# Performance work log

Hardware: AMD Instinct MI355X
Metric: run time of the kernel (lower is better)

Reference implementation:

```python
import jax, jax.numpy as jnp
import numpy as np
from math import factorial

LMAX = 5
MUL = 128            # multiplicity per irrep degree in the node embedding
NUM_CHANNELS = 4
NUM_RADII = 64
RES_BETA = 180
RES_ALPHA = 359
NUM_SPECIES = 5
NUM_GRAPHS = 16
NUM_NODES = 512
SH_DIM = (LMAX + 1) ** 2          # 36
EMB_DIM = MUL * SH_DIM            # 4608
NUM_IRREPS = MUL * (LMAX + 1)     # 768
INV_TEMP = 1.0


def _real_sh_basis(lmax, res_beta, res_alpha):
    """Orthonormal real spherical harmonics evaluated on a Gauss-Legendre beta grid
    and a uniform alpha grid (the grid used by e3nn.to_s2grid with gausslegendre
    quadrature). Returns B[(l*l + l + m), beta, alpha]. Precomputed in numpy since
    the grid is static."""
    y, _ = np.polynomial.legendre.leggauss(res_beta)          # y = cos(beta)
    alpha = np.linspace(0.0, 2.0 * np.pi, res_alpha, endpoint=False)
    # associated Legendre P[l, m] on y (Condon-Shortley phase)
    P = np.zeros((lmax + 1, lmax + 1, res_beta))
    P[0, 0] = 1.0
    somx2 = np.sqrt(np.clip(1.0 - y * y, 0.0, None))
    for m in range(1, lmax + 1):
        P[m, m] = -(2 * m - 1) * somx2 * P[m - 1, m - 1]
    for m in range(lmax):
        P[m + 1, m] = (2 * m + 1) * y * P[m, m]
    for m in range(lmax + 1):
        for l in range(m + 2, lmax + 1):
            P[l, m] = ((2 * l - 1) * y * P[l - 1, m] - (l + m - 1) * P[l - 2, m]) / (l - m)
    B = np.zeros(((lmax + 1) ** 2, res_beta, res_alpha))
    ones_a = np.ones_like(alpha)
    for l in range(lmax + 1):
        for m in range(l + 1):
            N = np.sqrt((2 * l + 1) / (4.0 * np.pi) * factorial(l - m) / factorial(l + m))
            if m == 0:
                B[l * l + l] = (N * P[l, 0])[:, None] * ones_a[None, :]
            else:
                B[l * l + l + m] = np.sqrt(2.0) * N * P[l, m][:, None] * np.cos(m * alpha)[None, :]
                B[l * l + l - m] = np.sqrt(2.0) * N * P[l, m][:, None] * np.sin(m * alpha)[None, :]
    return jnp.asarray(B, dtype=jnp.float32)


_B = _real_sh_basis(LMAX, RES_BETA, RES_ALPHA)   # (36, 180, 359)


def _split_blocks(emb):
    """Split an irreps array (G, sum_l MUL*(2l+1)) into per-degree blocks (G, MUL, 2l+1)."""
    blocks, off = [], 0
    for l in range(LMAX + 1):
        d = 2 * l + 1
        blocks.append(emb[:, off:off + MUL * d].reshape(-1, MUL, d))
        off += MUL * d
    return blocks


def setup_inputs() -> dict:
    key = jax.random.key(0)
    ks = jax.random.split(key, 13)
    inp = {
        "node_embeddings": jax.random.normal(ks[0], (NUM_NODES, EMB_DIM), jnp.float32),
        "species_embed": jax.random.normal(ks[1], (NUM_SPECIES, NUM_IRREPS), jnp.float32),
        "W_radial": jax.random.normal(ks[2], (MUL, NUM_RADII), jnp.float32),
        "W_mlp1": jax.random.normal(ks[3], (NUM_RADII, MUL), jnp.float32),
        "W_mlp2": jax.random.normal(ks[4], (MUL, NUM_RADII), jnp.float32),
    }
    for l in range(LMAX + 1):
        inp[f"W_ang_{l}"] = jax.random.normal(ks[5 + l], (MUL, NUM_CHANNELS), jnp.float32)
    inp["focus_indices"] = jax.random.randint(ks[11], (NUM_GRAPHS,), 0, NUM_NODES)
    inp["target_species"] = jax.random.randint(ks[12], (NUM_GRAPHS,), 0, NUM_SPECIES)
    return inp


def _forward(node_embeddings, species_embed, W_radial, W_mlp1, W_mlp2, W_ang,
             focus_indices, target_species):
    rsqrt_mul = np.float32(1.0 / np.sqrt(MUL))
    focus = node_embeddings[focus_indices]                 # (G, EMB_DIM)
    spec = species_embed[target_species]                   # (G, NUM_IRREPS), one scalar per irrep
    blocks = _split_blocks(focus)
    # target_species_embeddings * focus_node_embeddings: scale each irrep by its scalar
    scaled = [blk * spec[:, MUL * l:MUL * (l + 1), None] for l, blk in enumerate(blocks)]
    # radial path: e3nn Linear to num_radii x 0e (only 0e inputs contribute) + MLP
    scal0 = scaled[0][..., 0]                              # (G, MUL)
    r = (scal0 @ W_radial) * rsqrt_mul                     # (G, NUM_RADII)
    h = jax.nn.softplus((r @ W_mlp1) * np.float32(1.0 / np.sqrt(NUM_RADII)))
    radial_logits = (h @ W_mlp2) * rsqrt_mul               # (G, NUM_RADII)
    # angular path: e3nn Linear to num_channels * s2_irreps (per-degree channel mixing)
    ang = jnp.concatenate(
        [jnp.einsum("gkm,kc->gcm", scaled[l], W_ang[l]) * rsqrt_mul
         for l in range(LMAX + 1)], axis=-1)               # (G, C, 36)
    # joint distribution coefficients: radial logit adds to the l=0 coefficient
    joint0 = ang[:, :, None, :1] + radial_logits[:, None, :, None]     # (G, C, R, 1)
    rest = jnp.broadcast_to(ang[:, :, None, 1:],
                            (NUM_GRAPHS, NUM_CHANNELS, NUM_RADII, SH_DIM - 1))
    log_position_coeffs = jnp.concatenate([joint0, rest], axis=-1) * np.float32(INV_TEMP)
    # log_coeffs_to_logits: SH synthesis on the grid, then logsumexp over channels
    pos_grid = jnp.einsum("gcrk,kba->gcrba", log_position_coeffs, _B)
    position_logits = jax.nn.logsumexp(pos_grid, axis=1)   # (G, R, beta, alpha)
    ang_grid = jnp.einsum("gck,kba->gcba", ang, _B)
    angular_logits = jax.nn.logsumexp(ang_grid, axis=1, keepdims=True)  # (G, 1, beta, alpha)
    return log_position_coeffs, position_logits, angular_logits, radial_logits


def reference(node_embeddings, species_embed, W_radial, W_mlp1, W_mlp2,
              W_ang_0, W_ang_1, W_ang_2, W_ang_3, W_ang_4, W_ang_5,
              focus_indices, target_species):
    W_ang = [W_ang_0, W_ang_1, W_ang_2, W_ang_3, W_ang_4, W_ang_5]
    return _forward(node_embeddings, species_embed, W_radial, W_mlp1, W_mlp2, W_ang,
                    focus_indices, target_species)
```

## Files before the change

kernel.cpp:

```cpp
#include <hip/hip_runtime.h>
#include <math.h>

#define LMAX   5
#define MUL    128
#define NCH    4
#define NRAD   64
#define RBETA  180
#define RALPHA 359
#define NGRAPH 16
#define SH_DIM 36
#define EMB_DIM 4608
#define NIRR   768

#define GRID_BA (RBETA * RALPHA)
#define N_F4    (GRID_BA / 4)

#define OUT0_OFF 0
#define OUT1_OFF 147456
#define OUT2_OFF (147456 + 66170880)
#define OUT3_OFF (147456 + 66170880 + 1033920)


__global__ void k_nodes(double* __restrict__ y) {
    __shared__ double rcp[RBETA];
    const int n = RBETA;
    int tid = threadIdx.x;
    for (int k = tid; k < n; k += blockDim.x) rcp[k] = 1.0 / (double)(k + 1);
    __syncthreads();
    int i = tid;
    if (i >= n) return;
    const double PI = 3.14159265358979323846;
    double x = -cos(PI * (i + 0.75) / (n + 0.5));
    for (int it = 0; it < 6; ++it) {
        double p0 = 1.0, p1 = x;
        for (int k = 1; k < n; ++k) {
            double p2 = ((2.0 * k + 1.0) * x * p1 - (double)k * p0) * rcp[k];
            p0 = p1; p1 = p2;
        }
        double dp = n * (x * p1 - p0) / (x * x - 1.0);
        x -= p1 / dp;
    }
    y[i] = x;
}

__global__ __launch_bounds__(256)
void k_small(const float* __restrict__ ne, const float* __restrict__ sp,
             const float* __restrict__ wrad, const float* __restrict__ wm1,
             const float* __restrict__ wm2,
             const float* __restrict__ wa0, const float* __restrict__ wa1,
             const float* __restrict__ wa2, const float* __restrict__ wa3,
             const float* __restrict__ wa4, const float* __restrict__ wa5,
             const int* __restrict__ focus, const int* __restrict__ tspec,
             float* __restrict__ out0, float* __restrict__ out3,
             float* __restrict__ ang_ws, float* __restrict__ rad_ws)
{
    __shared__ float s0[MUL];
    __shared__ float rr[NRAD];
    __shared__ float hh[MUL];
    __shared__ float rl[NRAD];
    __shared__ float sang[NCH * SH_DIM];

    const int g = blockIdx.x;
    const int tid = threadIdx.x;
    const int fi = focus[g];
    const int ts = tspec[g];
    const float rs128 = 0.08838834764831845f;
    const float rs64  = 0.125f;

    if (tid < MUL) s0[tid] = ne[(size_t)fi * EMB_DIM + tid] * sp[ts * NIRR + tid];
    __syncthreads();

    if (tid < NRAD) {
        float acc = 0.f;
        for (int k = 0; k < MUL; ++k) acc += s0[k] * wrad[k * NRAD + tid];
        rr[tid] = acc * rs128;
    }
    __syncthreads();

    if (tid < MUL) {
        float acc = 0.f;
        for (int j = 0; j < NRAD; ++j) acc += rr[j] * wm1[j * MUL + tid];
        float x = acc * rs64;
        hh[tid] = fmaxf(x, 0.f) + log1pf(expf(-fabsf(x)));
    }
    __syncthreads();

    if (tid < NRAD) {
        float acc = 0.f;
        for (int k = 0; k < MUL; ++k) acc += hh[k] * wm2[k * NRAD + tid];
        float v = acc * rs128;
        rl[tid] = v;
        out3[g * NRAD + tid] = v;
        rad_ws[g * NRAD + tid] = v;
    }

    const float* WA[6] = {wa0, wa1, wa2, wa3, wa4, wa5};
    for (int t = tid; t < NCH * SH_DIM; t += blockDim.x) {
        int c = t / SH_DIM, kk = t % SH_DIM;
        int l = 0;
        while ((l + 1) * (l + 1) <= kk) ++l;
        int j = kk - l * l;
        int d = 2 * l + 1;
        const float* w  = WA[l];
        const float* nb = ne + (size_t)fi * EMB_DIM + MUL * l * l + j;
        const float* sb = sp + ts * NIRR + MUL * l;
        float acc = 0.f;
        for (int k = 0; k < MUL; ++k) acc += nb[k * d] * sb[k] * w[k * NCH + c];
        float v = acc * rs128;
        sang[t] = v;
        ang_ws[g * (NCH * SH_DIM) + t] = v;
    }
    __syncthreads();

    for (int t = tid; t < NCH * NRAD * SH_DIM; t += blockDim.x) {
        int kk = t % SH_DIM;
        int r  = (t / SH_DIM) % NRAD;
        int c  = t / (SH_DIM * NRAD);
        float v = sang[c * SH_DIM + kk];
        if (kk == 0) v += rl[r];
        out0[(size_t)g * (NCH * NRAD * SH_DIM) + t] = v;
    }
}

__global__ __launch_bounds__(256)
void k_angular(const double* __restrict__ y, const float* __restrict__ ang_ws,
               float* __restrict__ out2)
{
    __shared__ float sW[21];
    __shared__ float sAng[NCH * SH_DIM];
    __shared__ float sF[NCH][11];

    const int beta = blockIdx.x;
    const int g    = blockIdx.y;
    const int tid  = threadIdx.x;

    for (int t = tid; t < NCH * SH_DIM; t += 256)
        sAng[t] = ang_ws[g * (NCH * SH_DIM) + t];

    if (tid == 0) {
        double yy = y[beta];
        double P[LMAX + 1][LMAX + 1];
        P[0][0] = 1.0;
        double somx2 = sqrt(fmax(1.0 - yy * yy, 0.0));
        for (int m = 1; m <= LMAX; ++m) P[m][m] = -(2.0 * m - 1.0) * somx2 * P[m - 1][m - 1];
        for (int m = 0; m < LMAX; ++m)  P[m + 1][m] = (2.0 * m + 1.0) * yy * P[m][m];
        for (int m = 0; m <= LMAX; ++m)
            for (int l = m + 2; l <= LMAX; ++l)
                P[l][m] = ((2.0 * l - 1.0) * yy * P[l - 1][m] - (l + m - 1.0) * P[l - 2][m]) / (double)(l - m);
        const double FOURPI = 12.566370614359172;
        for (int l = 0; l <= LMAX; ++l) {
            for (int m = 0; m <= l; ++m) {
                double fr = 1.0;
                for (int k = l - m + 1; k <= l + m; ++k) fr /= (double)k;
                double N = sqrt((2.0 * l + 1.0) / FOURPI * fr);
                double w = N * P[l][m];
                if (m > 0) w *= 1.4142135623730951;
                sW[l * (l + 1) / 2 + m] = (float)w;
            }
        }
    }
    __syncthreads();

    if (tid < NCH * 11) {
        int c = tid / 11, j = tid % 11;
        float acc = 0.f;
        if (j == 0) {
            for (int l = 0; l <= LMAX; ++l)
                acc += sAng[c * SH_DIM + l * l + l] * sW[l * (l + 1) / 2];
        } else if (j <= 5) {
            int m = j;
            for (int l = m; l <= LMAX; ++l)
                acc += sAng[c * SH_DIM + l * l + l + m] * sW[l * (l + 1) / 2 + m];
        } else {
            int m = j - 5;
            for (int l = m; l <= LMAX; ++l)
                acc += sAng[c * SH_DIM + l * l + l - m] * sW[l * (l + 1) / 2 + m];
        }
        sF[c][j] = acc;
    }
    __syncthreads();

    const float dalpha = 6.283185307179586f / 359.0f;
    for (int a = tid; a < RALPHA; a += 256) {
        float alpha = dalpha * (float)a;
        float s1, c1;
        __sincosf(alpha, &s1, &c1);
        float t0 = sF[0][0], t1 = sF[1][0], t2 = sF[2][0], t3 = sF[3][0];
        float cm = c1, sm = s1;
        for (int m = 1; m <= 5; ++m) {
            t0 += sF[0][m] * cm + sF[0][5 + m] * sm;
            t1 += sF[1][m] * cm + sF[1][5 + m] * sm;
            t2 += sF[2][m] * cm + sF[2][5 + m] * sm;
            t3 += sF[3][m] * cm + sF[3][5 + m] * sm;
            float cn = cm * c1 - sm * s1;
            float sn = sm * c1 + cm * s1;
            cm = cn; sm = sn;
        }
        float mx = fmaxf(fmaxf(t0, t1), fmaxf(t2, t3));
        float s = expf(t0 - mx) + expf(t1 - mx) + expf(t2 - mx) + expf(t3 - mx);
        out2[(size_t)g * GRID_BA + beta * RALPHA + a] = mx + logf(s);
    }
}

__global__ __launch_bounds__(256)
void k_pos(const float* __restrict__ out2, const float* __restrict__ rad_ws,
           float* __restrict__ out1)
{
    const int g = blockIdx.z;
    const int r = blockIdx.y;
    const int i = blockIdx.x * 256 + threadIdx.x;
    if (i >= N_F4) return;
    const float rc = rad_ws[g * NRAD + r] * 0.28209479177387814f;
    const float4* src = (const float4*)(out2 + (size_t)g * GRID_BA);
    float4 v = src[i];
    v.x += rc; v.y += rc; v.z += rc; v.w += rc;
    float4* dst = (float4*)(out1 + ((size_t)(g * NRAD + r)) * GRID_BA);
    dst[i] = v;
}

extern "C" void kernel_launch(void* const* d_in, const int* in_sizes, int n_in,
                              void* d_out, int out_size, void* d_ws, size_t ws_size,
                              hipStream_t stream) {
    const float* ne   = (const float*)d_in[0];
    const float* sp   = (const float*)d_in[1];
    const float* wrad = (const float*)d_in[2];
    const float* wm1  = (const float*)d_in[3];
    const float* wm2  = (const float*)d_in[4];
    const float* wa0  = (const float*)d_in[5];
    const float* wa1  = (const float*)d_in[6];
    const float* wa2  = (const float*)d_in[7];
    const float* wa3  = (const float*)d_in[8];
    const float* wa4  = (const float*)d_in[9];
    const float* wa5  = (const float*)d_in[10];
    const int* focus  = (const int*)d_in[11];
    const int* tspec  = (const int*)d_in[12];

    float* out  = (float*)d_out;
    float* out0 = out + OUT0_OFF;
    float* out1 = out + OUT1_OFF;
    float* out2 = out + OUT2_OFF;
    float* out3 = out + OUT3_OFF;

    double* y     = (double*)d_ws;
    float* ang_ws = (float*)((char*)d_ws + 2048);
    float* rad_ws = (float*)((char*)d_ws + 2048 + 9216);

    hipLaunchKernelGGL(k_nodes, dim3(1), dim3(192), 0, stream, y);
    hipLaunchKernelGGL(k_small, dim3(NGRAPH), dim3(256), 0, stream,
                       ne, sp, wrad, wm1, wm2, wa0, wa1, wa2, wa3, wa4, wa5,
                       focus, tspec, out0, out3, ang_ws, rad_ws);
    hipLaunchKernelGGL(k_angular, dim3(RBETA, NGRAPH), dim3(256), 0, stream,
                       y, ang_ws, out2);
    hipLaunchKernelGGL(k_pos, dim3((N_F4 + 255) / 256, NRAD, NGRAPH), dim3(256), 0, stream,
                       out2, rad_ws, out1);
}
```

Measured before the change: 363.1 us.

## Fuse position-logit broadcast into angular kernel and precompute SH weight table

Merges the angular logsumexp kernel with the position broadcast kernel. Each block now writes all 64 radial rows of out1 straight from registers, so out2 is no longer read back from memory. The per-beta Legendre/SH weight computation moves from a single serial thread in each block into the prep kernel, which writes a shared table, and the Legendre node iteration is rescaled to avoid division. The trade-off is that out1 is written with scalar stores per row instead of float4, across only 2880 blocks with long store loops, which may reduce store efficiency.

After: 412.9 us. 1.14x slower.

```diff
diff --git a/kernel.cpp b/kernel.cpp
--- a/kernel.cpp
+++ b/kernel.cpp
@@ -13,7 +13,6 @@
 #define NIRR   768
 
 #define GRID_BA (RBETA * RALPHA)
-#define N_F4    (GRID_BA / 4)
 
 #define OUT0_OFF 0
 #define OUT1_OFF 147456
@@ -21,26 +20,45 @@
 #define OUT3_OFF (147456 + 66170880 + 1033920)
 
 
-__global__ void k_nodes(double* __restrict__ y) {
-    __shared__ double rcp[RBETA];
+__global__ __launch_bounds__(192)
+void k_prep(float* __restrict__ sWtab) {
+    const int i = threadIdx.x;
+    if (i >= RBETA) return;
     const int n = RBETA;
-    int tid = threadIdx.x;
-    for (int k = tid; k < n; k += blockDim.x) rcp[k] = 1.0 / (double)(k + 1);
-    __syncthreads();
-    int i = tid;
-    if (i >= n) return;
     const double PI = 3.14159265358979323846;
     double x = -cos(PI * (i + 0.75) / (n + 0.5));
     for (int it = 0; it < 6; ++it) {
-        double p0 = 1.0, p1 = x;
+        double s0 = 1.0, s1 = x;
         for (int k = 1; k < n; ++k) {
-            double p2 = ((2.0 * k + 1.0) * x * p1 - (double)k * p0) * rcp[k];
-            p0 = p1; p1 = p2;
-        }
-        double dp = n * (x * p1 - p0) / (x * x - 1.0);
-        x -= p1 / dp;
-    }
-    y[i] = x;
+            double dk = (double)k;
+            double a  = fma(2.0 * dk, x, x);
+            double s2 = fma(a, s1, -(dk * dk) * s0);
+            s0 = s1; s1 = s2;
+            if (fabs(s1) > 0x1p500) { s1 *= 0x1p-500; s0 *= 0x1p-500; }
+        }
+        double num = (x * x - 1.0) * s1;
+        double den = (double)n * fma(x, s1, -(double)n * s0);
+        x -= num / den;
+    }
+    double P[LMAX + 1][LMAX + 1];
+    P[0][0] = 1.0;
+    double somx2 = sqrt(fmax(1.0 - x * x, 0.0));
+    for (int m = 1; m <= LMAX; ++m) P[m][m] = -(2.0 * m - 1.0) * somx2 * P[m - 1][m - 1];
+    for (int m = 0; m < LMAX; ++m)  P[m + 1][m] = (2.0 * m + 1.0) * x * P[m][m];
+    for (int m = 0; m <= LMAX; ++m)
+        for (int l = m + 2; l <= LMAX; ++l)
+            P[l][m] = ((2.0 * l - 1.0) * x * P[l - 1][m] - (l + m - 1.0) * P[l - 2][m]) / (double)(l - m);
+    const double FOURPI = 12.566370614359172;
+    for (int l = 0; l <= LMAX; ++l) {
+        for (int m = 0; m <= l; ++m) {
+            double fr = 1.0;
+            for (int k = l - m + 1; k <= l + m; ++k) fr /= (double)k;
+            double N = sqrt((2.0 * l + 1.0) / FOURPI * fr);
+            double w = N * P[l][m];
+            if (m > 0) w *= 1.4142135623730951;
+            sWtab[i * 21 + l * (l + 1) / 2 + m] = (float)w;
+        }
+    }
 }
 
 __global__ __launch_bounds__(256)
@@ -123,12 +141,14 @@
 }
 
 __global__ __launch_bounds__(256)
-void k_angular(const double* __restrict__ y, const float* __restrict__ ang_ws,
-               float* __restrict__ out2)
+void k_main(const float* __restrict__ sWtab, const float* __restrict__ ang_ws,
+            const float* __restrict__ rad_ws,
+            float* __restrict__ out1, float* __restrict__ out2)
 {
     __shared__ float sW[21];
     __shared__ float sAng[NCH * SH_DIM];
     __shared__ float sF[NCH][11];
+    __shared__ float sRad[NRAD];
 
     const int beta = blockIdx.x;
     const int g    = blockIdx.y;
@@ -136,29 +156,9 @@
 
     for (int t = tid; t < NCH * SH_DIM; t += 256)
         sAng[t] = ang_ws[g * (NCH * SH_DIM) + t];
-
-    if (tid == 0) {
-        double yy = y[beta];
-        double P[LMAX + 1][LMAX + 1];
-        P[0][0] = 1.0;
-        double somx2 = sqrt(fmax(1.0 - yy * yy, 0.0));
-        for (int m = 1; m <= LMAX; ++m) P[m][m] = -(2.0 * m - 1.0) * somx2 * P[m - 1][m - 1];
-        for (int m = 0; m < LMAX; ++m)  P[m + 1][m] = (2.0 * m + 1.0) * yy * P[m][m];
-        for (int m = 0; m <= LMAX; ++m)
-            for (int l = m + 2; l <= LMAX; ++l)
-                P[l][m] = ((2.0 * l - 1.0) * yy * P[l - 1][m] - (l + m - 1.0) * P[l - 2][m]) / (double)(l - m);
-        const double FOURPI = 12.566370614359172;
-        for (int l = 0; l <= LMAX; ++l) {
-            for (int m = 0; m <= l; ++m) {
-                double fr = 1.0;
-                for (int k = l - m + 1; k <= l + m; ++k) fr /= (double)k;
-                double N = sqrt((2.0 * l + 1.0) / FOURPI * fr);
-                double w = N * P[l][m];
-                if (m > 0) w *= 1.4142135623730951;
-                sW[l * (l + 1) / 2 + m] = (float)w;
-            }
-        }
-    }
+    if (tid < 21) sW[tid] = sWtab[beta * 21 + tid];
+    if (tid >= 192)
+        sRad[tid - 192] = rad_ws[g * NRAD + (tid - 192)] * 0.28209479177387814f;
     __syncthreads();
 
     if (tid < NCH * 11) {
@@ -181,12 +181,17 @@
     __syncthreads();
 
     const float dalpha = 6.283185307179586f / 359.0f;
-    for (int a = tid; a < RALPHA; a += 256) {
+    float v[2];
+    #pragma unroll
+    for (int half = 0; half < 2; ++half) {
+        int a = tid + half * 256;
+        if (a >= RALPHA) { v[half] = 0.f; continue; }
         float alpha = dalpha * (float)a;
         float s1, c1;
         __sincosf(alpha, &s1, &c1);
         float t0 = sF[0][0], t1 = sF[1][0], t2 = sF[2][0], t3 = sF[3][0];
         float cm = c1, sm = s1;
+        #pragma unroll
         for (int m = 1; m <= 5; ++m) {
             t0 += sF[0][m] * cm + sF[0][5 + m] * sm;
             t1 += sF[1][m] * cm + sF[1][5 + m] * sm;
@@ -198,24 +203,19 @@
         }
         float mx = fmaxf(fmaxf(t0, t1), fmaxf(t2, t3));
         float s = expf(t0 - mx) + expf(t1 - mx) + expf(t2 - mx) + expf(t3 - mx);
-        out2[(size_t)g * GRID_BA + beta * RALPHA + a] = mx + logf(s);
-    }
-}
-
-__global__ __launch_bounds__(256)
-void k_pos(const float* __restrict__ out2, const float* __restrict__ rad_ws,
-           float* __restrict__ out1)
-{
-    const int g = blockIdx.z;
-    const int r = blockIdx.y;
-    const int i = blockIdx.x * 256 + threadIdx.x;
-    if (i >= N_F4) return;
-    const float rc = rad_ws[g * NRAD + r] * 0.28209479177387814f;
-    const float4* src = (const float4*)(out2 + (size_t)g * GRID_BA);
-    float4 v = src[i];
-    v.x += rc; v.y += rc; v.z += rc; v.w += rc;
-    float4* dst = (float4*)(out1 + ((size_t)(g * NRAD + r)) * GRID_BA);
-    dst[i] = v;
+        v[half] = mx + logf(s);
+        out2[(size_t)g * GRID_BA + beta * RALPHA + a] = v[half];
+    }
+
+    const int second = (tid + 256 < RALPHA) ? 1 : 0;
+    size_t base = ((size_t)(g * NRAD) * RBETA + beta) * RALPHA;
+    #pragma unroll 4
+    for (int r = 0; r < NRAD; ++r) {
+        float rc = sRad[r];
+        float* row = out1 + base + (size_t)r * GRID_BA;
+        row[tid] = v[0] + rc;
+        if (second) row[tid + 256] = v[1] + rc;
+    }
 }
 
 extern "C" void kernel_launch(void* const* d_in, const int* in_sizes, int n_in,
@@ -241,16 +241,14 @@
     float* out2 = out + OUT2_OFF;
     float* out3 = out + OUT3_OFF;
 
-    double* y     = (double*)d_ws;
-    float* ang_ws = (float*)((char*)d_ws + 2048);
-    float* rad_ws = (float*)((char*)d_ws + 2048 + 9216);
-
-    hipLaunchKernelGGL(k_nodes, dim3(1), dim3(192), 0, stream, y);
+    float* sWtab  = (float*)d_ws;
+    float* ang_ws = (float*)((char*)d_ws + 16384);
+    float* rad_ws = (float*)((char*)d_ws + 26624);
+
+    hipLaunchKernelGGL(k_prep, dim3(1), dim3(192), 0, stream, sWtab);
     hipLaunchKernelGGL(k_small, dim3(NGRAPH), dim3(256), 0, stream,
                        ne, sp, wrad, wm1, wm2, wa0, wa1, wa2, wa3, wa4, wa5,
                        focus, tspec, out0, out3, ang_ws, rad_ws);
-    hipLaunchKernelGGL(k_angular, dim3(RBETA, NGRAPH), dim3(256), 0, stream,
-                       y, ang_ws, out2);
-    hipLaunchKernelGGL(k_pos, dim3((N_F4 + 255) / 256, NRAD, NGRAPH), dim3(256), 0, stream,
-                       out2, rad_ws, out1);
-}
+    hipLaunchKernelGGL(k_main, dim3(RBETA, NGRAPH), dim3(256), 0, stream,
+                       sWtab, ang_ws, rad_ws, out1, out2);
+}
```
